# Performance work log

Hardware: AMD Instinct MI355X
Metric: run time of the kernel (lower is better)

Reference implementation:

```python
import jax, jax.numpy as jnp
import numpy as np

N = 50000          # nodes
E = 800000         # edges
D_IN, D_HID, D_OUT = 256, 128, 64
NUM_GRAPHS = 16
BN_EPS = 1e-5


def gcn_conv(x, src, dst, W, b, n_nodes):
    """PyG GCNConv: add self-loops, sym-normalized aggregation, then bias."""
    loop = jnp.arange(n_nodes, dtype=src.dtype)
    s = jnp.concatenate([src, loop])
    d = jnp.concatenate([dst, loop])
    deg = jax.ops.segment_sum(jnp.ones_like(s, dtype=x.dtype), d, num_segments=n_nodes)
    dinv = jax.lax.rsqrt(jnp.maximum(deg, 1.0))  # deg >= 1 due to self-loops
    norm = dinv[s] * dinv[d]                      # [E+N]
    h = x @ W                                     # [N, out]
    msg = h[s] * norm[:, None]                    # gather + scale
    out = jax.ops.segment_sum(msg, d, num_segments=n_nodes)
    return out + b


def batch_norm(x, gamma, beta):
    mu = jnp.mean(x, axis=0)
    var = jnp.mean(jnp.square(x - mu), axis=0)
    return (x - mu) * jax.lax.rsqrt(var + BN_EPS) * gamma + beta


def setup_inputs() -> dict:
    key = jax.random.key(0)
    ks = jax.random.split(key, 10)
    x = jax.random.normal(ks[0], (N, D_IN), dtype=jnp.float32)
    edge_index = jax.random.randint(ks[1], (2, E), 0, N, dtype=jnp.int64)
    batch = jnp.sort(jax.random.randint(ks[2], (N,), 0, NUM_GRAPHS, dtype=jnp.int64))
    def glorot(k, fan_in, fan_out):
        lim = np.sqrt(6.0 / (fan_in + fan_out))
        return jax.random.uniform(k, (fan_in, fan_out), jnp.float32, -lim, lim)
    return {
        "x": x, "edge_index": edge_index, "batch": batch,
        "W1": glorot(ks[3], D_IN, D_HID),  "b1": jnp.zeros((D_HID,), jnp.float32),
        "W2": glorot(ks[4], D_HID, D_HID), "b2": jnp.zeros((D_HID,), jnp.float32),
        "W3": glorot(ks[5], D_HID, D_OUT), "b3": jnp.zeros((D_OUT,), jnp.float32),
        "g1": jnp.ones((D_HID,), jnp.float32), "be1": jnp.zeros((D_HID,), jnp.float32),
        "g2": jnp.ones((D_HID,), jnp.float32), "be2": jnp.zeros((D_HID,), jnp.float32),
    }


def reference(x, edge_index, batch, W1, b1, W2, b2, W3, b3, g1, be1, g2, be2):
    src, dst = edge_index[0], edge_index[1]
    n = x.shape[0]
    h = gcn_conv(x, src, dst, W1, b1, n)
    h = jax.nn.relu(batch_norm(h, g1, be1))
    h = gcn_conv(h, src, dst, W2, b2, n)
    h = jax.nn.relu(batch_norm(h, g2, be2))
    h = gcn_conv(h, src, dst, W3, b3, n)          # [N, D_OUT]
    # global mean pool over graph ids
    sums = jax.ops.segment_sum(h, batch, num_segments=NUM_GRAPHS)
    cnts = jax.ops.segment_sum(jnp.ones((n,), h.dtype), batch, num_segments=NUM_GRAPHS)
    return sums / jnp.maximum(cnts, 1.0)[:, None]  # [NUM_GRAPHS, D_OUT]
```

## Files before the change

### kernel.cpp

```cpp
#include <hip/hip_runtime.h>
#include <hip/hip_bf16.h>

#define D_IN   256
#define D_HID  128
#define D_OUT_ 64
#define NGRAPH 16
#define BN_EPS 1e-5f

#define SCAN_TPB 256
#define SCAN_VPT 4

typedef __attribute__((ext_vector_type(8))) short short8;
typedef __attribute__((ext_vector_type(4))) float floatx4;

__device__ __forceinline__ unsigned short f2bf(float x) {
    unsigned u = __float_as_uint(x);
    return (unsigned short)((u + 0x7fffu + ((u >> 16) & 1u)) >> 16);
}
__device__ __forceinline__ unsigned pack2bf(float lo, float hi) {
    return (unsigned)f2bf(lo) | ((unsigned)f2bf(hi) << 16);
}
__device__ __forceinline__ void bf2_decode(unsigned u, float& lo, float& hi) {
    lo = __uint_as_float(u << 16);
    hi = __uint_as_float(u & 0xffff0000u);
}
__device__ __forceinline__ void accum8(float* acc, uint4 qv, float wt) {
    float f0,f1,f2,f3,f4,f5,f6,f7;
    bf2_decode(qv.x, f0, f1); bf2_decode(qv.y, f2, f3);
    bf2_decode(qv.z, f4, f5); bf2_decode(qv.w, f6, f7);
    acc[0]=fmaf(f0,wt,acc[0]); acc[1]=fmaf(f1,wt,acc[1]);
    acc[2]=fmaf(f2,wt,acc[2]); acc[3]=fmaf(f3,wt,acc[3]);
    acc[4]=fmaf(f4,wt,acc[4]); acc[5]=fmaf(f5,wt,acc[5]);
    acc[6]=fmaf(f6,wt,acc[6]); acc[7]=fmaf(f7,wt,acc[7]);
}

__global__ void count_rank_kernel(const int* __restrict__ dst, int E,
                                  int* __restrict__ deg, int* __restrict__ rank) {
    int e0 = blockIdx.x * (256 * 4) + threadIdx.x;
    int d[4];
    #pragma unroll
    for (int i = 0; i < 4; ++i) {
        int e = e0 + i * 256;
        if (e < E) d[i] = dst[e];
    }
    #pragma unroll
    for (int i = 0; i < 4; ++i) {
        int e = e0 + i * 256;
        if (e < E) rank[e] = atomicAdd(&deg[d[i]], 1);
    }
}

__global__ void dinv_bsum_kernel(const int* __restrict__ deg, int N,
                                 float* __restrict__ dinv, int* __restrict__ bsum) {
    __shared__ int red[SCAN_TPB];
    int t = threadIdx.x;
    int base = blockIdx.x * (SCAN_TPB * SCAN_VPT) + t;
    int s = 0;
    #pragma unroll
    for (int i = 0; i < SCAN_VPT; ++i) {
        int idx = base + i * SCAN_TPB;
        if (idx < N) {
            int d = deg[idx];
            dinv[idx] = rsqrtf((float)(d + 1));
            s += d;
        }
    }
    red[t] = s;
    __syncthreads();
    for (int off = SCAN_TPB / 2; off > 0; off >>= 1) {
        if (t < off) red[t] += red[t + off];
        __syncthreads();
    }
    if (t == 0) bsum[blockIdx.x] = red[0];
}

__global__ void scan_bsum_kernel(const int* __restrict__ bsum, int NB,
                                 int* __restrict__ bprefix,
                                 int* __restrict__ rowstart, int N, int E) {
    __shared__ int part[SCAN_TPB];
    int t = threadIdx.x;
    int s = (t < NB) ? bsum[t] : 0;
    part[t] = s;
    __syncthreads();
    for (int off = 1; off < SCAN_TPB; off <<= 1) {
        int x = (t >= off) ? part[t - off] : 0;
        __syncthreads();
        part[t] += x;
        __syncthreads();
    }
    if (t < NB) bprefix[t] = part[t] - s;
    if (t == 0) rowstart[N] = E;
}

__global__ void local_scan_kernel(const int* __restrict__ deg, int N,
                                  const int* __restrict__ bprefix,
                                  int* __restrict__ rowstart) {
    __shared__ int part[SCAN_TPB];
    int t = threadIdx.x;
    int base = blockIdx.x * (SCAN_TPB * SCAN_VPT) + t * SCAN_VPT;
    int v[SCAN_VPT];
    int s = 0;
    #pragma unroll
    for (int i = 0; i < SCAN_VPT; ++i) {
        v[i] = (base + i < N) ? deg[base + i] : 0;
        s += v[i];
    }
    part[t] = s;
    __syncthreads();
    for (int off = 1; off < SCAN_TPB; off <<= 1) {
        int x = (t >= off) ? part[t - off] : 0;
        __syncthreads();
        part[t] += x;
        __syncthreads();
    }
    int excl = part[t] - s + bprefix[blockIdx.x];
    #pragma unroll
    for (int i = 0; i < SCAN_VPT; ++i) {
        if (base + i < N) rowstart[base + i] = excl;
        excl += v[i];
    }
}

__global__ void scatter_kernel(const int* __restrict__ src, const int* __restrict__ dst,
                               int E, const int* __restrict__ rowstart,
                               const int* __restrict__ rank, int* __restrict__ csr) {
    int e0 = blockIdx.x * (256 * 4) + threadIdx.x;
    int d[4], rk[4], sv[4], pos[4];
    #pragma unroll
    for (int i = 0; i < 4; ++i) {
        int e = e0 + i * 256;
        if (e < E) { d[i] = dst[e]; rk[i] = rank[e]; sv[i] = src[e]; }
    }
    #pragma unroll
    for (int i = 0; i < 4; ++i) {
        int e = e0 + i * 256;
        if (e < E) pos[i] = rowstart[d[i]];
    }
    #pragma unroll
    for (int i = 0; i < 4; ++i) {
        int e = e0 + i * 256;
        if (e < E) csr[pos[i] + rk[i]] = sv[i];
    }
}

__global__ void wprep_all_kernel(const float* __restrict__ W1, const float* __restrict__ W2,
                                 const float* __restrict__ W3,
                                 unsigned short* __restrict__ Wt1,
                                 unsigned short* __restrict__ Wt2,
                                 unsigned short* __restrict__ Wt3) {
    int idx = blockIdx.x * blockDim.x + threadIdx.x;
    const int S1 = D_IN * D_HID;
    const int S2 = D_HID * D_HID;
    const int S3 = D_HID * D_OUT_;
    if (idx < S1) {
        int k = idx / D_HID, n = idx - k * D_HID;
        Wt1[(size_t)n * D_IN + k] = f2bf(W1[idx]);
    } else if (idx < S1 + S2) {
        int i = idx - S1;
        int k = i / D_HID, n = i - k * D_HID;
        Wt2[(size_t)n * D_HID + k] = f2bf(W2[i]);
    } else if (idx < S1 + S2 + S3) {
        int i = idx - S1 - S2;
        int k = i / D_OUT_, n = i - k * D_OUT_;
        Wt3[(size_t)n * D_HID + k] = f2bf(W3[i]);
    }
}

template<int K, int NOUT, int FUSE, int ABF16>
__device__ __forceinline__ void gemm_body(
        int bid, const void* __restrict__ Aptr, const unsigned short* __restrict__ Wt,
        unsigned short* __restrict__ Cb, int M,
        const float* __restrict__ sums, const float* __restrict__ sumsq,
        const float* __restrict__ gam, const float* __restrict__ bet, float invN) {
    constexpr int NT = NOUT / 16;
    constexpr int KS = K / 32;
    constexpr int CHUNKS = NOUT * K / 8;
    constexpr int KROW16 = K / 8;
    __shared__ unsigned short s_wt[NOUT * K];
    __shared__ float s_sc[FUSE ? K : 1];
    __shared__ float s_sh[FUSE ? K : 1];

    int lane = threadIdx.x & 63;
    int wave = threadIdx.x >> 6;
    int col  = lane & 15;
    int quad = lane >> 4;
    int kq   = quad * 8;
    int row  = bid * 64 + wave * 16 + col;
    int rowc = min(row, M - 1);

    uint4  qa[ABF16 ? KS : 1];
    float4 a0[ABF16 ? 1 : KS], a1[ABF16 ? 1 : KS];
    if (ABF16) {
        const unsigned short* Ab = (const unsigned short*)Aptr;
        #pragma unroll
        for (int i = 0; i < KS; ++i)
            qa[i] = *(const uint4*)&Ab[(size_t)rowc * K + i * 32 + kq];
    } else {
        const float* Af = (const float*)Aptr;
        #pragma unroll
        for (int i = 0; i < KS; ++i) {
            a0[i] = *(const float4*)&Af[(size_t)rowc * K + i * 32 + kq];
            a1[i] = *(const float4*)&Af[(size_t)rowc * K + i * 32 + kq + 4];
        }
    }

    {
        const uint4* Wg = (const uint4*)Wt;
        #pragma unroll
        for (int it = 0; it < CHUNKS / 256; ++it) {
            int c = it * 256 + (int)threadIdx.x;
            uint4 v = Wg[c];
            int n = c / KROW16;
            unsigned byte = ((unsigned)c * 16u) ^ ((unsigned)(n & 7) << 4);
            *(uint4*)((char*)s_wt + byte) = v;
        }
    }
    if (FUSE) {
        int t = threadIdx.x;
        if (t < K) {
            float mu  = sums[t] * invN;
            float var = sumsq[t] * invN - mu * mu;
            float sc  = gam[t] * rsqrtf(var + BN_EPS);
            s_sc[t] = sc;
            s_sh[t] = fmaf(-mu, sc, bet[t]);
        }
    }
    __syncthreads();

    short8 afr[KS];
    if (ABF16) {
        #pragma unroll
        for (int i = 0; i < KS; ++i) {
            if (FUSE) {
                int kb = i * 32 + kq;
                float f0,f1,f2,f3,f4,f5,f6,f7;
                bf2_decode(qa[i].x, f0, f1); bf2_decode(qa[i].y, f2, f3);
                bf2_decode(qa[i].z, f4, f5); bf2_decode(qa[i].w, f6, f7);
                float4 sc0 = *(const float4*)&s_sc[kb];
                float4 sc1 = *(const float4*)&s_sc[kb + 4];
                float4 sh0 = *(const float4*)&s_sh[kb];
                float4 sh1 = *(const float4*)&s_sh[kb + 4];
                f0 = fmaxf(0.f, fmaf(f0, sc0.x, sh0.x));
                f1 = fmaxf(0.f, fmaf(f1, sc0.y, sh0.y));
                f2 = fmaxf(0.f, fmaf(f2, sc0.z, sh0.z));
                f3 = fmaxf(0.f, fmaf(f3, sc0.w, sh0.w));
                f4 = fmaxf(0.f, fmaf(f4, sc1.x, sh1.x));
                f5 = fmaxf(0.f, fmaf(f5, sc1.y, sh1.y));
                f6 = fmaxf(0.f, fmaf(f6, sc1.z, sh1.z));
                f7 = fmaxf(0.f, fmaf(f7, sc1.w, sh1.w));
                uint4 p;
                p.x = pack2bf(f0, f1); p.y = pack2bf(f2, f3);
                p.z = pack2bf(f4, f5); p.w = pack2bf(f6, f7);
                afr[i] = __builtin_bit_cast(short8, p);
            } else {
                afr[i] = __builtin_bit_cast(short8, qa[i]);
            }
        }
    } else {
        #pragma unroll
        for (int i = 0; i < KS; ++i) {
            uint4 p;
            p.x = pack2bf(a0[i].x, a0[i].y); p.y = pack2bf(a0[i].z, a0[i].w);
            p.z = pack2bf(a1[i].x, a1[i].y); p.w = pack2bf(a1[i].z, a1[i].w);
            afr[i] = __builtin_bit_cast(short8, p);
        }
    }

    floatx4 acc[NT];
    #pragma unroll
    for (int nt = 0; nt < NT; ++nt) acc[nt] = (floatx4){0.f, 0.f, 0.f, 0.f};

    #pragma unroll
    for (int i = 0; i < KS; ++i) {
        #pragma unroll
        for (int nt = 0; nt < NT; ++nt) {
            unsigned byte = ((unsigned)((nt * 16 + col) * K + i * 32 + kq)) * 2u;
            byte ^= (unsigned)(col & 7) << 4;
            short8 bfrag = *(const short8*)((const char*)s_wt + byte);
            acc[nt] = __builtin_amdgcn_mfma_f32_16x16x32_bf16(afr[i], bfrag, acc[nt], 0, 0, 0);
        }
    }

    int obase = bid * 64 + wave * 16 + quad * 4;
    #pragma unroll
    for (int r = 0; r < 4; ++r) {
        int orow = obase + r;
        if (orow < M) {
            #pragma unroll
            for (int nt = 0; nt < NT; ++nt)
                Cb[(size_t)orow * NOUT + nt * 16 + col] = f2bf(acc[nt][r]);
        }
    }
}

template<int K, int NOUT, int FUSE, int ABF16>
__global__ __launch_bounds__(256, 2) void gemm_mfma_kernel(
        const void* __restrict__ Aptr, const unsigned short* __restrict__ Wt,
        unsigned short* __restrict__ Cb, int M,
        const float* __restrict__ sums, const float* __restrict__ sumsq,
        const float* __restrict__ gam, const float* __restrict__ bet, float invN) {
    gemm_body<K, NOUT, FUSE, ABF16>(blockIdx.x, Aptr, Wt, Cb, M, sums, sumsq, gam, bet, invN);
}

template<int D>
__global__ __launch_bounds__(256) void agg_bf16_kernel(
        const unsigned short* __restrict__ h, const float* __restrict__ dinv,
        const int* __restrict__ rowstart, const int* __restrict__ csr,
        const float* __restrict__ bias,
        unsigned short* __restrict__ outb, int N) {
    constexpr int LPR = D / 8;
    constexpr int RPB = 256 / LPR;
    int lane = threadIdx.x & (LPR - 1);
    int r    = threadIdx.x / LPR;
    int v = blockIdx.x * RPB + r;
    if (v >= N) return;
    int c0 = lane * 8;
    const unsigned short* hc = h + c0;
    float dv = dinv[v];

    float acc[8];
    {
        float w = dv * dv;
        uint4 q = *(const uint4*)&hc[(size_t)v * D];
        float4 b0 = *(const float4*)&bias[c0];
        float4 b1 = *(const float4*)&bias[c0 + 4];
        acc[0]=b0.x; acc[1]=b0.y; acc[2]=b0.z; acc[3]=b0.w;
        acc[4]=b1.x; acc[5]=b1.y; acc[6]=b1.z; acc[7]=b1.w;
        accum8(acc, q, w);
    }

    int j  = rowstart[v];
    int j1 = rowstart[v + 1];
    for (; j + 8 <= j1; j += 8) {
        int   s[8]; float w[8]; uint4 q[8];
        #pragma unroll
        for (int i = 0; i < 8; ++i) s[i] = csr[j + i];
        #pragma unroll
        for (int i = 0; i < 8; ++i) q[i] = *(const uint4*)&hc[(size_t)s[i] * D];
        #pragma unroll
        for (int i = 0; i < 8; ++i) w[i] = dinv[s[i]] * dv;
        #pragma unroll
        for (int i = 0; i < 8; ++i) accum8(acc, q[i], w[i]);
    }
    for (; j + 4 <= j1; j += 4) {
        int s0 = csr[j],     s1 = csr[j + 1];
        int s2 = csr[j + 2], s3 = csr[j + 3];
        float w0 = dinv[s0] * dv, w1 = dinv[s1] * dv;
        float w2 = dinv[s2] * dv, w3 = dinv[s3] * dv;
        uint4 q0 = *(const uint4*)&hc[(size_t)s0 * D];
        uint4 q1 = *(const uint4*)&hc[(size_t)s1 * D];
        uint4 q2 = *(const uint4*)&hc[(size_t)s2 * D];
        uint4 q3 = *(const uint4*)&hc[(size_t)s3 * D];
        accum8(acc, q0, w0); accum8(acc, q1, w1);
        accum8(acc, q2, w2); accum8(acc, q3, w3);
    }
    for (; j < j1; ++j) {
        int s = csr[j];
        float w = dinv[s] * dv;
        uint4 q = *(const uint4*)&hc[(size_t)s * D];
        accum8(acc, q, w);
    }

    uint4 o;
    o.x = pack2bf(acc[0], acc[1]); o.y = pack2bf(acc[2], acc[3]);
    o.z = pack2bf(acc[4], acc[5]); o.w = pack2bf(acc[6], acc[7]);
    *(uint4*)&outb[(size_t)v * D + c0] = o;
}

__global__ void bn_stats_bf16_kernel(const unsigned short* __restrict__ x, int N,
                                     float* __restrict__ sums, float* __restrict__ sumsq) {
    __shared__ float ls0[256], ls1[256], lq0[256], lq1[256];
    int pr = threadIdx.x & 63;
    int rg = threadIdx.x >> 6;
    float s0=0.f, s1=0.f, q0=0.f, q1=0.f;
    for (int v = blockIdx.x * 4 + rg; v < N; v += gridDim.x * 4) {
        unsigned u = *(const unsigned*)&x[(size_t)v * 128 + pr * 2];
        float lo, hi; bf2_decode(u, lo, hi);
        s0 += lo; s1 += hi;
        q0 = fmaf(lo, lo, q0); q1 = fmaf(hi, hi, q1);
    }
    ls0[threadIdx.x]=s0; ls1[threadIdx.x]=s1; lq0[threadIdx.x]=q0; lq1[threadIdx.x]=q1;
    __syncthreads();
    if (threadIdx.x < 64) {
        int pp = threadIdx.x;
        float a0=0,a1=0,b0=0,b1=0;
        #pragma unroll
        for (int g = 0; g < 4; ++g) {
            a0 += ls0[g*64+pp]; a1 += ls1[g*64+pp];
            b0 += lq0[g*64+pp]; b1 += lq1[g*64+pp];
        }
        atomicAdd(&sums[pp*2],  a0); atomicAdd(&sums[pp*2+1],  a1);
        atomicAdd(&sumsq[pp*2], b0); atomicAdd(&sumsq[pp*2+1], b1);
    }
}

__global__ void pool_bf16_kernel(const unsigned short* __restrict__ x,
                                 const int* __restrict__ batch, int N,
                                 float* __restrict__ psum, int* __restrict__ pcnt) {
    __shared__ float ls[NGRAPH * 64];
    __shared__ int   lc[NGRAPH];
    for (int i = threadIdx.x; i < NGRAPH * 64; i += blockDim.x) ls[i] = 0.f;
    if (threadIdx.x < NGRAPH) lc[threadIdx.x] = 0;
    __syncthreads();
    int total = N * 32;
    for (int idx = blockIdx.x * blockDim.x + threadIdx.x; idx < total;
         idx += gridDim.x * blockDim.x) {
        int v = idx >> 5, cp = idx & 31;
        unsigned u = *(const unsigned*)&x[(size_t)v * 64 + cp * 2];
        float lo, hi; bf2_decode(u, lo, hi);
        int g = batch[v];
        atomicAdd(&ls[g * 64 + cp * 2],     lo);
        atomicAdd(&ls[g * 64 + cp * 2 + 1], hi);
        if (cp == 0) atomicAdd(&lc[g], 1);
    }
    __syncthreads();
    for (int i = threadIdx.x; i < NGRAPH * 64; i += blockDim.x) atomicAdd(&psum[i], ls[i]);
    if (threadIdx.x < NGRAPH) atomicAdd(&pcnt[threadIdx.x], lc[threadIdx.x]);
}

__global__ void pool_final_kernel(const float* __restrict__ psum, const int* __restrict__ pcnt,
                                  float* __restrict__ out) {
    int i = threadIdx.x;
    int g = i >> 6;
    float cnt = (float)max(pcnt[g], 1);
    out[i] = psum[i] / cnt;
}

extern "C" void kernel_launch(void* const* d_in, const int* in_sizes, int n_in,
                              void* d_out, int out_size, void* d_ws, size_t ws_size,
                              hipStream_t stream) {
    const float* x   = (const float*)d_in[0];
    const int*   ei  = (const int*)d_in[1];
    const int*   bat = (const int*)d_in[2];
    const float* W1  = (const float*)d_in[3];
    const float* b1  = (const float*)d_in[4];
    const float* W2  = (const float*)d_in[5];
    const float* b2  = (const float*)d_in[6];
    const float* W3  = (const float*)d_in[7];
    const float* b3  = (const float*)d_in[8];
    const float* g1  = (const float*)d_in[9];
    const float* be1 = (const float*)d_in[10];
    const float* g2  = (const float*)d_in[11];
    const float* be2 = (const float*)d_in[12];
    float* out = (float*)d_out;

    int N = in_sizes[0] / D_IN;
    int E = in_sizes[1] / 2;
    const int* src = ei;
    const int* dst = ei + E;

    char* p = (char*)d_ws;
    auto alloc = [&](size_t bytes) { char* r = p; p += (bytes + 255) & ~(size_t)255; return r; };
    int NB = (N + SCAN_TPB * SCAN_VPT - 1) / (SCAN_TPB * SCAN_VPT);
    char*  zbase    = p;
    int*   deg      = (int*)  alloc((size_t)N * 4);
    float* sums1    = (float*)alloc(128 * 4);
    float* sumsq1   = (float*)alloc(128 * 4);
    float* sums2    = (float*)alloc(128 * 4);
    float* sumsq2   = (float*)alloc(128 * 4);
    float* psum     = (float*)alloc(NGRAPH * 64 * 4);
    int*   pcnt     = (int*)  alloc(NGRAPH * 4);
    size_t zspan    = (size_t)(p - zbase);
    int*   rowstart = (int*)  alloc((size_t)(N + 1) * 4);
    int*   rank     = (int*)  alloc((size_t)E * 4);
    float* dinv     = (float*)alloc((size_t)N * 4);
    int*   bsum     = (int*)  alloc((size_t)NB * 4);
    int*   bprefix  = (int*)  alloc((size_t)NB * 4);
    int*   csr      = (int*)  alloc((size_t)E * 4);
    unsigned short* hb16   = (unsigned short*)alloc((size_t)N * 128 * 2);
    unsigned short* aggb16 = (unsigned short*)alloc((size_t)N * 128 * 2);
    unsigned short* Wt1 = (unsigned short*)alloc((size_t)D_HID * D_IN * 2);
    unsigned short* Wt2 = (unsigned short*)alloc((size_t)D_HID * D_HID * 2);
    unsigned short* Wt3 = (unsigned short*)alloc((size_t)D_OUT_ * D_HID * 2);

    int ebl4 = (E + 1023) / 1024;
    int gblocks = (N + 63) / 64;
    float invN = 1.0f / (float)N;
    int wtot = D_IN * D_HID + D_HID * D_HID + D_HID * D_OUT_;

    (void)hipMemsetAsync(zbase, 0, zspan, stream);
    wprep_all_kernel<<<(wtot + 255) / 256, 256, 0, stream>>>(W1, W2, W3, Wt1, Wt2, Wt3);

    count_rank_kernel<<<ebl4, 256, 0, stream>>>(dst, E, deg, rank);
    dinv_bsum_kernel<<<NB, SCAN_TPB, 0, stream>>>(deg, N, dinv, bsum);
    scan_bsum_kernel<<<1, SCAN_TPB, 0, stream>>>(bsum, NB, bprefix, rowstart, N, E);
    local_scan_kernel<<<NB, SCAN_TPB, 0, stream>>>(deg, N, bprefix, rowstart);
    scatter_kernel<<<ebl4, 256, 0, stream>>>(src, dst, E, rowstart, rank, csr);

    gemm_mfma_kernel<D_IN, D_HID, 0, 0><<<gblocks, 256, 0, stream>>>(
        x, Wt1, hb16, N, nullptr, nullptr, nullptr, nullptr, 0.f);

    agg_bf16_kernel<D_HID><<<(N + 15) / 16, 256, 0, stream>>>(
        hb16, dinv, rowstart, csr, b1, aggb16, N);
    bn_stats_bf16_kernel<<<256, 256, 0, stream>>>(aggb16, N, sums1, sumsq1);

    gemm_mfma_kernel<D_HID, D_HID, 1, 1><<<gblocks, 256, 0, stream>>>(
        aggb16, Wt2, hb16, N, sums1, sumsq1, g1, be1, invN);
    agg_bf16_kernel<D_HID><<<(N + 15) / 16, 256, 0, stream>>>(
        hb16, dinv, rowstart, csr, b2, aggb16, N);
    bn_stats_bf16_kernel<<<256, 256, 0, stream>>>(aggb16, N, sums2, sumsq2);

    gemm_mfma_kernel<D_HID, D_OUT_, 1, 1><<<gblocks, 256, 0, stream>>>(
        aggb16, Wt3, hb16, N, sums2, sumsq2, g2, be2, invN);
    agg_bf16_kernel<D_OUT_><<<(N + 31) / 32, 256, 0, stream>>>(
        hb16, dinv, rowstart, csr, b3, aggb16, N);

    pool_bf16_kernel<<<256, 256, 0, stream>>>(aggb16, bat, N, psum, pcnt);
    pool_final_kernel<<<1, NGRAPH * 64, 0, stream>>>(psum, pcnt, out);
}
```

Baseline: 357.0 us.

## Fuse CSR build, BN stats and pooling into neighbouring kernels

Weight prep is merged with degree counting in one launch. The per-edge rank array is replaced by an atomic cursor, and that scatter shares a launch with the first GEMM. BN statistics and global mean pooling move into the aggregation kernels' epilogues, so the separate stats and pool passes and the final bf16 output write are dropped. This cuts launches and memory re-reads, but CSR neighbour order becomes nondeterministic, which changes float summation order, and more global atomics are added per block.

```diff
diff --git a/kernel.cpp b/kernel.cpp
--- a/kernel.cpp
+++ b/kernel.cpp
@@ -34,19 +34,43 @@
     acc[6]=fmaf(f6,wt,acc[6]); acc[7]=fmaf(f7,wt,acc[7]);
 }
 
-__global__ void count_rank_kernel(const int* __restrict__ dst, int E,
-                                  int* __restrict__ deg, int* __restrict__ rank) {
-    int e0 = blockIdx.x * (256 * 4) + threadIdx.x;
-    int d[4];
-    #pragma unroll
-    for (int i = 0; i < 4; ++i) {
-        int e = e0 + i * 256;
-        if (e < E) d[i] = dst[e];
-    }
-    #pragma unroll
-    for (int i = 0; i < 4; ++i) {
-        int e = e0 + i * 256;
-        if (e < E) rank[e] = atomicAdd(&deg[d[i]], 1);
+__global__ void prep_count_kernel(const float* __restrict__ W1, const float* __restrict__ W2,
+                                  const float* __restrict__ W3,
+                                  unsigned short* __restrict__ Wt1,
+                                  unsigned short* __restrict__ Wt2,
+                                  unsigned short* __restrict__ Wt3, int WB,
+                                  const int* __restrict__ dst, int E,
+                                  int* __restrict__ deg) {
+    if ((int)blockIdx.x < WB) {
+        int idx = blockIdx.x * 256 + threadIdx.x;
+        const int S1 = D_IN * D_HID;
+        const int S2 = D_HID * D_HID;
+        const int S3 = D_HID * D_OUT_;
+        if (idx < S1) {
+            int k = idx / D_HID, n = idx - k * D_HID;
+            Wt1[(size_t)n * D_IN + k] = f2bf(W1[idx]);
+        } else if (idx < S1 + S2) {
+            int i = idx - S1;
+            int k = i / D_HID, n = i - k * D_HID;
+            Wt2[(size_t)n * D_HID + k] = f2bf(W2[i]);
+        } else if (idx < S1 + S2 + S3) {
+            int i = idx - S1 - S2;
+            int k = i / D_OUT_, n = i - k * D_OUT_;
+            Wt3[(size_t)n * D_HID + k] = f2bf(W3[i]);
+        }
+    } else {
+        int e0 = ((int)blockIdx.x - WB) * (256 * 4) + threadIdx.x;
+        int d[4];
+        #pragma unroll
+        for (int i = 0; i < 4; ++i) {
+            int e = e0 + i * 256;
+            if (e < E) d[i] = dst[e];
+        }
+        #pragma unroll
+        for (int i = 0; i < 4; ++i) {
+            int e = e0 + i * 256;
+            if (e < E) atomicAdd(&deg[d[i]], 1);
+        }
     }
 }
 
@@ -94,7 +118,7 @@
 
 __global__ void local_scan_kernel(const int* __restrict__ deg, int N,
                                   const int* __restrict__ bprefix,
-                                  int* __restrict__ rowstart) {
+                                  int* __restrict__ rowstart, int* __restrict__ cursor) {
     __shared__ int part[SCAN_TPB];
     int t = threadIdx.x;
     int base = blockIdx.x * (SCAN_TPB * SCAN_VPT) + t * SCAN_VPT;
@@ -116,53 +140,8 @@
     int excl = part[t] - s + bprefix[blockIdx.x];
     #pragma unroll
     for (int i = 0; i < SCAN_VPT; ++i) {
-        if (base + i < N) rowstart[base + i] = excl;
+        if (base + i < N) { rowstart[base + i] = excl; cursor[base + i] = excl; }
         excl += v[i];
-    }
-}
-
-__global__ void scatter_kernel(const int* __restrict__ src, const int* __restrict__ dst,
-                               int E, const int* __restrict__ rowstart,
-                               const int* __restrict__ rank, int* __restrict__ csr) {
-    int e0 = blockIdx.x * (256 * 4) + threadIdx.x;
-    int d[4], rk[4], sv[4], pos[4];
-    #pragma unroll
-    for (int i = 0; i < 4; ++i) {
-        int e = e0 + i * 256;
-        if (e < E) { d[i] = dst[e]; rk[i] = rank[e]; sv[i] = src[e]; }
-    }
-    #pragma unroll
-    for (int i = 0; i < 4; ++i) {
-        int e = e0 + i * 256;
-        if (e < E) pos[i] = rowstart[d[i]];
-    }
-    #pragma unroll
-    for (int i = 0; i < 4; ++i) {
-        int e = e0 + i * 256;
-        if (e < E) csr[pos[i] + rk[i]] = sv[i];
-    }
-}
-
-__global__ void wprep_all_kernel(const float* __restrict__ W1, const float* __restrict__ W2,
-                                 const float* __restrict__ W3,
-                                 unsigned short* __restrict__ Wt1,
-                                 unsigned short* __restrict__ Wt2,
-                                 unsigned short* __restrict__ Wt3) {
-    int idx = blockIdx.x * blockDim.x + threadIdx.x;
-    const int S1 = D_IN * D_HID;
-    const int S2 = D_HID * D_HID;
-    const int S3 = D_HID * D_OUT_;
-    if (idx < S1) {
-        int k = idx / D_HID, n = idx - k * D_HID;
-        Wt1[(size_t)n * D_IN + k] = f2bf(W1[idx]);
-    } else if (idx < S1 + S2) {
-        int i = idx - S1;
-        int k = i / D_HID, n = i - k * D_HID;
-        Wt2[(size_t)n * D_HID + k] = f2bf(W2[i]);
-    } else if (idx < S1 + S2 + S3) {
-        int i = idx - S1 - S2;
-        int k = i / D_OUT_, n = i - k * D_OUT_;
-        Wt3[(size_t)n * D_HID + k] = f2bf(W3[i]);
     }
 }
 
@@ -302,26 +281,71 @@
     gemm_body<K, NOUT, FUSE, ABF16>(blockIdx.x, Aptr, Wt, Cb, M, sums, sumsq, gam, bet, invN);
 }
 
-template<int D>
+__global__ __launch_bounds__(256, 2) void gemm1_scatter_kernel(
+        const float* __restrict__ x, const unsigned short* __restrict__ Wt1,
+        unsigned short* __restrict__ Cb, int M, int GB,
+        const int* __restrict__ src, const int* __restrict__ dst, int E,
+        int* __restrict__ cursor, int* __restrict__ csr) {
+    if ((int)blockIdx.x < GB) {
+        gemm_body<D_IN, D_HID, 0, 0>(blockIdx.x, x, Wt1, Cb, M,
+                                     nullptr, nullptr, nullptr, nullptr, 0.f);
+    } else {
+        int e0 = ((int)blockIdx.x - GB) * (256 * 4) + threadIdx.x;
+        int d[4], sv[4];
+        #pragma unroll
+        for (int i = 0; i < 4; ++i) {
+            int e = e0 + i * 256;
+            if (e < E) { d[i] = dst[e]; sv[i] = src[e]; }
+        }
+        #pragma unroll
+        for (int i = 0; i < 4; ++i) {
+            int e = e0 + i * 256;
+            if (e < E) {
+                int pos = atomicAdd(&cursor[d[i]], 1);
+                csr[pos] = sv[i];
+            }
+        }
+    }
+}
+
+template<int D, int BNS, int POOL>
 __global__ __launch_bounds__(256) void agg_bf16_kernel(
         const unsigned short* __restrict__ h, const float* __restrict__ dinv,
         const int* __restrict__ rowstart, const int* __restrict__ csr,
         const float* __restrict__ bias,
-        unsigned short* __restrict__ outb, int N) {
+        unsigned short* __restrict__ outb, int N,
+        float* __restrict__ sums, float* __restrict__ sumsq,
+        const int* __restrict__ batch, float* __restrict__ psum,
+        int* __restrict__ pcnt) {
+    static_assert(!BNS || D == 128, "BNS reduce assumes LPR=16 (4 rows/wave)");
     constexpr int LPR = D / 8;
     constexpr int RPB = 256 / LPR;
+    __shared__ float s_ps[BNS ? 4 : 1][BNS ? 128 : 1];
+    __shared__ float s_pq[BNS ? 4 : 1][BNS ? 128 : 1];
+    __shared__ float s_pool[POOL ? NGRAPH : 1][POOL ? 64 : 1];
+    __shared__ int   s_cnt[POOL ? NGRAPH : 1];
+    __shared__ int   s_gmin, s_gmax;
+
+    if (POOL) {
+        for (int i = threadIdx.x; i < NGRAPH * 64; i += 256) (&s_pool[0][0])[i] = 0.f;
+        if (threadIdx.x < NGRAPH) s_cnt[threadIdx.x] = 0;
+        if (threadIdx.x == 0) { s_gmin = NGRAPH - 1; s_gmax = 0; }
+        __syncthreads();
+    }
+
     int lane = threadIdx.x & (LPR - 1);
     int r    = threadIdx.x / LPR;
     int v = blockIdx.x * RPB + r;
-    if (v >= N) return;
+    bool valid = v < N;
+    int vc = valid ? v : N - 1;
     int c0 = lane * 8;
     const unsigned short* hc = h + c0;
-    float dv = dinv[v];
+    float dv = dinv[vc];
 
     float acc[8];
     {
         float w = dv * dv;
-        uint4 q = *(const uint4*)&hc[(size_t)v * D];
+        uint4 q = *(const uint4*)&hc[(size_t)vc * D];
         float4 b0 = *(const float4*)&bias[c0];
         float4 b1 = *(const float4*)&bias[c0 + 4];
         acc[0]=b0.x; acc[1]=b0.y; acc[2]=b0.z; acc[3]=b0.w;
@@ -329,8 +353,8 @@
         accum8(acc, q, w);
     }
 
-    int j  = rowstart[v];
-    int j1 = rowstart[v + 1];
+    int j  = rowstart[vc];
+    int j1 = valid ? rowstart[vc + 1] : j;
     for (; j + 8 <= j1; j += 8) {
         int   s[8]; float w[8]; uint4 q[8];
         #pragma unroll
@@ -361,61 +385,63 @@
         accum8(acc, q, w);
     }
 
-    uint4 o;
-    o.x = pack2bf(acc[0], acc[1]); o.y = pack2bf(acc[2], acc[3]);
-    o.z = pack2bf(acc[4], acc[5]); o.w = pack2bf(acc[6], acc[7]);
-    *(uint4*)&outb[(size_t)v * D + c0] = o;
-}
-
-__global__ void bn_stats_bf16_kernel(const unsigned short* __restrict__ x, int N,
-                                     float* __restrict__ sums, float* __restrict__ sumsq) {
-    __shared__ float ls0[256], ls1[256], lq0[256], lq1[256];
-    int pr = threadIdx.x & 63;
-    int rg = threadIdx.x >> 6;
-    float s0=0.f, s1=0.f, q0=0.f, q1=0.f;
-    for (int v = blockIdx.x * 4 + rg; v < N; v += gridDim.x * 4) {
-        unsigned u = *(const unsigned*)&x[(size_t)v * 128 + pr * 2];
-        float lo, hi; bf2_decode(u, lo, hi);
-        s0 += lo; s1 += hi;
-        q0 = fmaf(lo, lo, q0); q1 = fmaf(hi, hi, q1);
-    }
-    ls0[threadIdx.x]=s0; ls1[threadIdx.x]=s1; lq0[threadIdx.x]=q0; lq1[threadIdx.x]=q1;
-    __syncthreads();
-    if (threadIdx.x < 64) {
-        int pp = threadIdx.x;
-        float a0=0,a1=0,b0=0,b1=0;
-        #pragma unroll
-        for (int g = 0; g < 4; ++g) {
-            a0 += ls0[g*64+pp]; a1 += ls1[g*64+pp];
-            b0 += lq0[g*64+pp]; b1 += lq1[g*64+pp];
-        }
-        atomicAdd(&sums[pp*2],  a0); atomicAdd(&sums[pp*2+1],  a1);
-        atomicAdd(&sumsq[pp*2], b0); atomicAdd(&sumsq[pp*2+1], b1);
-    }
-}
-
-__global__ void pool_bf16_kernel(const unsigned short* __restrict__ x,
-                                 const int* __restrict__ batch, int N,
-                                 float* __restrict__ psum, int* __restrict__ pcnt) {
-    __shared__ float ls[NGRAPH * 64];
-    __shared__ int   lc[NGRAPH];
-    for (int i = threadIdx.x; i < NGRAPH * 64; i += blockDim.x) ls[i] = 0.f;
-    if (threadIdx.x < NGRAPH) lc[threadIdx.x] = 0;
-    __syncthreads();
-    int total = N * 32;
-    for (int idx = blockIdx.x * blockDim.x + threadIdx.x; idx < total;
-         idx += gridDim.x * blockDim.x) {
-        int v = idx >> 5, cp = idx & 31;
-        unsigned u = *(const unsigned*)&x[(size_t)v * 64 + cp * 2];
-        float lo, hi; bf2_decode(u, lo, hi);
-        int g = batch[v];
-        atomicAdd(&ls[g * 64 + cp * 2],     lo);
-        atomicAdd(&ls[g * 64 + cp * 2 + 1], hi);
-        if (cp == 0) atomicAdd(&lc[g], 1);
-    }
-    __syncthreads();
-    for (int i = threadIdx.x; i < NGRAPH * 64; i += blockDim.x) atomicAdd(&psum[i], ls[i]);
-    if (threadIdx.x < NGRAPH) atomicAdd(&pcnt[threadIdx.x], lc[threadIdx.x]);
+    if (!POOL && valid) {
+        uint4 o;
+        o.x = pack2bf(acc[0], acc[1]); o.y = pack2bf(acc[2], acc[3]);
+        o.z = pack2bf(acc[4], acc[5]); o.w = pack2bf(acc[6], acc[7]);
+        *(uint4*)&outb[(size_t)v * D + c0] = o;
+    }
+
+    if (BNS) {
+        float s[8], q2[8];
+        #pragma unroll
+        for (int i = 0; i < 8; ++i) {
+            s[i]  = valid ? acc[i] : 0.f;
+            q2[i] = valid ? acc[i] * acc[i] : 0.f;
+        }
+        #pragma unroll
+        for (int i = 0; i < 8; ++i) {
+            s[i]  += __shfl_xor(s[i], 16);  s[i]  += __shfl_xor(s[i], 32);
+            q2[i] += __shfl_xor(q2[i], 16); q2[i] += __shfl_xor(q2[i], 32);
+        }
+        int wv = threadIdx.x >> 6;
+        if ((threadIdx.x & 48) == 0) {
+            int l = threadIdx.x & 15;
+            #pragma unroll
+            for (int i = 0; i < 8; ++i) {
+                s_ps[wv][l * 8 + i] = s[i];
+                s_pq[wv][l * 8 + i] = q2[i];
+            }
+        }
+        __syncthreads();
+        int t = threadIdx.x;
+        if (t < 128) {
+            float vv = s_ps[0][t] + s_ps[1][t] + s_ps[2][t] + s_ps[3][t];
+            atomicAdd(&sums[t], vv);
+        } else {
+            int ch = t - 128;
+            float vv = s_pq[0][ch] + s_pq[1][ch] + s_pq[2][ch] + s_pq[3][ch];
+            atomicAdd(&sumsq[ch], vv);
+        }
+    }
+
+    if (POOL) {
+        if (valid) {
+            int g = batch[v];
+            #pragma unroll
+            for (int i = 0; i < 8; ++i) atomicAdd(&s_pool[g][c0 + i], acc[i]);
+            if (lane == 0) {
+                atomicAdd(&s_cnt[g], 1);
+                atomicMin(&s_gmin, g);
+                atomicMax(&s_gmax, g);
+            }
+        }
+        __syncthreads();
+        for (int g = s_gmin; g <= s_gmax; ++g)
+            if (threadIdx.x < 64) atomicAdd(&psum[g * 64 + threadIdx.x], s_pool[g][threadIdx.x]);
+        if (threadIdx.x < NGRAPH && s_cnt[threadIdx.x] > 0)
+            atomicAdd(&pcnt[threadIdx.x], s_cnt[threadIdx.x]);
+    }
 }
 
 __global__ void pool_final_kernel(const float* __restrict__ psum, const int* __restrict__ pcnt,
@@ -462,7 +488,7 @@
     int*   pcnt     = (int*)  alloc(NGRAPH * 4);
     size_t zspan    = (size_t)(p - zbase);
     int*   rowstart = (int*)  alloc((size_t)(N + 1) * 4);
-    int*   rank     = (int*)  alloc((size_t)E * 4);
+    int*   cursor   = (int*)  alloc((size_t)N * 4);
     float* dinv     = (float*)alloc((size_t)N * 4);
     int*   bsum     = (int*)  alloc((size_t)NB * 4);
     int*   bprefix  = (int*)  alloc((size_t)NB * 4);
@@ -477,34 +503,31 @@
     int gblocks = (N + 63) / 64;
     float invN = 1.0f / (float)N;
     int wtot = D_IN * D_HID + D_HID * D_HID + D_HID * D_OUT_;
+    int WB = (wtot + 255) / 256;
 
     (void)hipMemsetAsync(zbase, 0, zspan, stream);
-    wprep_all_kernel<<<(wtot + 255) / 256, 256, 0, stream>>>(W1, W2, W3, Wt1, Wt2, Wt3);
-
-    count_rank_kernel<<<ebl4, 256, 0, stream>>>(dst, E, deg, rank);
+    prep_count_kernel<<<WB + ebl4, 256, 0, stream>>>(W1, W2, W3, Wt1, Wt2, Wt3,
+                                                     WB, dst, E, deg);
+
     dinv_bsum_kernel<<<NB, SCAN_TPB, 0, stream>>>(deg, N, dinv, bsum);
     scan_bsum_kernel<<<1, SCAN_TPB, 0, stream>>>(bsum, NB, bprefix, rowstart, N, E);
-    local_scan_kernel<<<NB, SCAN_TPB, 0, stream>>>(deg, N, bprefix, rowstart);
-    scatter_kernel<<<ebl4, 256, 0, stream>>>(src, dst, E, rowstart, rank, csr);
-
-    gemm_mfma_kernel<D_IN, D_HID, 0, 0><<<gblocks, 256, 0, stream>>>(
-        x, Wt1, hb16, N, nullptr, nullptr, nullptr, nullptr, 0.f);
-
-    agg_bf16_kernel<D_HID><<<(N + 15) / 16, 256, 0, stream>>>(
-        hb16, dinv, rowstart, csr, b1, aggb16, N);
-    bn_stats_bf16_kernel<<<256, 256, 0, stream>>>(aggb16, N, sums1, sumsq1);
+    local_scan_kernel<<<NB, SCAN_TPB, 0, stream>>>(deg, N, bprefix, rowstart, cursor);
+
+    gemm1_scatter_kernel<<<gblocks + ebl4, 256, 0, stream>>>(
+        x, Wt1, hb16, N, gblocks, src, dst, E, cursor, csr);
+
+    agg_bf16_kernel<D_HID, 1, 0><<<(N + 15) / 16, 256, 0, stream>>>(
+        hb16, dinv, rowstart, csr, b1, aggb16, N, sums1, sumsq1, nullptr, nullptr, nullptr);
 
     gemm_mfma_kernel<D_HID, D_HID, 1, 1><<<gblocks, 256, 0, stream>>>(
         aggb16, Wt2, hb16, N, sums1, sumsq1, g1, be1, invN);
-    agg_bf16_kernel<D_HID><<<(N + 15) / 16, 256, 0, stream>>>(
-        hb16, dinv, rowstart, csr, b2, aggb16, N);
-    bn_stats_bf16_kernel<<<256, 256, 0, stream>>>(aggb16, N, sums2, sumsq2);
+    agg_bf16_kernel<D_HID, 1, 0><<<(N + 15) / 16, 256, 0, stream>>>(
+        hb16, dinv, rowstart, csr, b2, aggb16, N, sums2, sumsq2, nullptr, nullptr, nullptr);
 
     gemm_mfma_kernel<D_HID, D_OUT_, 1, 1><<<gblocks, 256, 0, stream>>>(
         aggb16, Wt3, hb16, N, sums2, sumsq2, g2, be2, invN);
-    agg_bf16_kernel<D_OUT_><<<(N + 31) / 32, 256, 0, stream>>>(
-        hb16, dinv, rowstart, csr, b3, aggb16, N);
-
-    pool_bf16_kernel<<<256, 256, 0, stream>>>(aggb16, bat, N, psum, pcnt);
+    agg_bf16_kernel<D_OUT_, 0, 1><<<(N + 31) / 32, 256, 0, stream>>>(
+        hb16, dinv, rowstart, csr, b3, nullptr, N, nullptr, nullptr, bat, psum, pcnt);
+
     pool_final_kernel<<<1, NGRAPH * 64, 0, stream>>>(psum, pcnt, out);
 }
```

New measurement: 466.5 us. 30.7% more time.

## Fuse weight prep with degree count and overlap CSR scatter with first GEMM

Applied to the files above, without the earlier changes.

Merges the weight transpose/convert kernel with the degree-count kernel into one launch, and merges the CSR scatter with the first GEMM through block-index partitioning so the two independent stages run concurrently. The scatter now takes positions from a per-node atomic cursor initialised from the scan, so the per-edge rank array and its extra read and write pass are gone. This removes two kernel launches and some memory traffic. In exchange, the order of neighbours within each CSR row becomes nondeterministic, which changes floating-point summation order, and the scatter blocks must share the GPU with GEMM blocks that run at launch bounds (256,2).

```diff
diff --git a/kernel.cpp b/kernel.cpp
--- a/kernel.cpp
+++ b/kernel.cpp
@@ -34,19 +34,43 @@
     acc[6]=fmaf(f6,wt,acc[6]); acc[7]=fmaf(f7,wt,acc[7]);
 }
 
-__global__ void count_rank_kernel(const int* __restrict__ dst, int E,
-                                  int* __restrict__ deg, int* __restrict__ rank) {
-    int e0 = blockIdx.x * (256 * 4) + threadIdx.x;
-    int d[4];
-    #pragma unroll
-    for (int i = 0; i < 4; ++i) {
-        int e = e0 + i * 256;
-        if (e < E) d[i] = dst[e];
-    }
-    #pragma unroll
-    for (int i = 0; i < 4; ++i) {
-        int e = e0 + i * 256;
-        if (e < E) rank[e] = atomicAdd(&deg[d[i]], 1);
+__global__ void prep_count_kernel(const float* __restrict__ W1, const float* __restrict__ W2,
+                                  const float* __restrict__ W3,
+                                  unsigned short* __restrict__ Wt1,
+                                  unsigned short* __restrict__ Wt2,
+                                  unsigned short* __restrict__ Wt3, int WB,
+                                  const int* __restrict__ dst, int E,
+                                  int* __restrict__ deg) {
+    if ((int)blockIdx.x < WB) {
+        int idx = blockIdx.x * 256 + threadIdx.x;
+        const int S1 = D_IN * D_HID;
+        const int S2 = D_HID * D_HID;
+        const int S3 = D_HID * D_OUT_;
+        if (idx < S1) {
+            int k = idx / D_HID, n = idx - k * D_HID;
+            Wt1[(size_t)n * D_IN + k] = f2bf(W1[idx]);
+        } else if (idx < S1 + S2) {
+            int i = idx - S1;
+            int k = i / D_HID, n = i - k * D_HID;
+            Wt2[(size_t)n * D_HID + k] = f2bf(W2[i]);
+        } else if (idx < S1 + S2 + S3) {
+            int i = idx - S1 - S2;
+            int k = i / D_OUT_, n = i - k * D_OUT_;
+            Wt3[(size_t)n * D_HID + k] = f2bf(W3[i]);
+        }
+    } else {
+        int e0 = ((int)blockIdx.x - WB) * (256 * 4) + threadIdx.x;
+        int d[4];
+        #pragma unroll
+        for (int i = 0; i < 4; ++i) {
+            int e = e0 + i * 256;
+            if (e < E) d[i] = dst[e];
+        }
+        #pragma unroll
+        for (int i = 0; i < 4; ++i) {
+            int e = e0 + i * 256;
+            if (e < E) atomicAdd(&deg[d[i]], 1);
+        }
     }
 }
 
@@ -94,7 +118,7 @@
 
 __global__ void local_scan_kernel(const int* __restrict__ deg, int N,
                                   const int* __restrict__ bprefix,
-                                  int* __restrict__ rowstart) {
+                                  int* __restrict__ rowstart, int* __restrict__ cursor) {
     __shared__ int part[SCAN_TPB];
     int t = threadIdx.x;
     int base = blockIdx.x * (SCAN_TPB * SCAN_VPT) + t * SCAN_VPT;
@@ -116,53 +140,8 @@
     int excl = part[t] - s + bprefix[blockIdx.x];
     #pragma unroll
     for (int i = 0; i < SCAN_VPT; ++i) {
-        if (base + i < N) rowstart[base + i] = excl;
+        if (base + i < N) { rowstart[base + i] = excl; cursor[base + i] = excl; }
         excl += v[i];
-    }
-}
-
-__global__ void scatter_kernel(const int* __restrict__ src, const int* __restrict__ dst,
-                               int E, const int* __restrict__ rowstart,
-                               const int* __restrict__ rank, int* __restrict__ csr) {
-    int e0 = blockIdx.x * (256 * 4) + threadIdx.x;
-    int d[4], rk[4], sv[4], pos[4];
-    #pragma unroll
-    for (int i = 0; i < 4; ++i) {
-        int e = e0 + i * 256;
-        if (e < E) { d[i] = dst[e]; rk[i] = rank[e]; sv[i] = src[e]; }
-    }
-    #pragma unroll
-    for (int i = 0; i < 4; ++i) {
-        int e = e0 + i * 256;
-        if (e < E) pos[i] = rowstart[d[i]];
-    }
-    #pragma unroll
-    for (int i = 0; i < 4; ++i) {
-        int e = e0 + i * 256;
-        if (e < E) csr[pos[i] + rk[i]] = sv[i];
-    }
-}
-
-__global__ void wprep_all_kernel(const float* __restrict__ W1, const float* __restrict__ W2,
-                                 const float* __restrict__ W3,
-                                 unsigned short* __restrict__ Wt1,
-                                 unsigned short* __restrict__ Wt2,
-                                 unsigned short* __restrict__ Wt3) {
-    int idx = blockIdx.x * blockDim.x + threadIdx.x;
-    const int S1 = D_IN * D_HID;
-    const int S2 = D_HID * D_HID;
-    const int S3 = D_HID * D_OUT_;
-    if (idx < S1) {
-        int k = idx / D_HID, n = idx - k * D_HID;
-        Wt1[(size_t)n * D_IN + k] = f2bf(W1[idx]);
-    } else if (idx < S1 + S2) {
-        int i = idx - S1;
-        int k = i / D_HID, n = i - k * D_HID;
-        Wt2[(size_t)n * D_HID + k] = f2bf(W2[i]);
-    } else if (idx < S1 + S2 + S3) {
-        int i = idx - S1 - S2;
-        int k = i / D_OUT_, n = i - k * D_OUT_;
-        Wt3[(size_t)n * D_HID + k] = f2bf(W3[i]);
     }
 }
 
@@ -302,6 +281,33 @@
     gemm_body<K, NOUT, FUSE, ABF16>(blockIdx.x, Aptr, Wt, Cb, M, sums, sumsq, gam, bet, invN);
 }
 
+__global__ __launch_bounds__(256, 2) void gemm1_scatter_kernel(
+        const float* __restrict__ x, const unsigned short* __restrict__ Wt1,
+        unsigned short* __restrict__ Cb, int M, int GB,
+        const int* __restrict__ src, const int* __restrict__ dst, int E,
+        int* __restrict__ cursor, int* __restrict__ csr) {
+    if ((int)blockIdx.x < GB) {
+        gemm_body<D_IN, D_HID, 0, 0>(blockIdx.x, x, Wt1, Cb, M,
+                                     nullptr, nullptr, nullptr, nullptr, 0.f);
+    } else {
+        int e0 = ((int)blockIdx.x - GB) * (256 * 4) + threadIdx.x;
+        int d[4], sv[4];
+        #pragma unroll
+        for (int i = 0; i < 4; ++i) {
+            int e = e0 + i * 256;
+            if (e < E) { d[i] = dst[e]; sv[i] = src[e]; }
+        }
+        #pragma unroll
+        for (int i = 0; i < 4; ++i) {
+            int e = e0 + i * 256;
+            if (e < E) {
+                int pos = atomicAdd(&cursor[d[i]], 1);
+                csr[pos] = sv[i];
+            }
+        }
+    }
+}
+
 template<int D>
 __global__ __launch_bounds__(256) void agg_bf16_kernel(
         const unsigned short* __restrict__ h, const float* __restrict__ dinv,
@@ -462,7 +468,7 @@
     int*   pcnt     = (int*)  alloc(NGRAPH * 4);
     size_t zspan    = (size_t)(p - zbase);
     int*   rowstart = (int*)  alloc((size_t)(N + 1) * 4);
-    int*   rank     = (int*)  alloc((size_t)E * 4);
+    int*   cursor   = (int*)  alloc((size_t)N * 4);
     float* dinv     = (float*)alloc((size_t)N * 4);
     int*   bsum     = (int*)  alloc((size_t)NB * 4);
     int*   bprefix  = (int*)  alloc((size_t)NB * 4);
@@ -477,18 +483,18 @@
     int gblocks = (N + 63) / 64;
     float invN = 1.0f / (float)N;
     int wtot = D_IN * D_HID + D_HID * D_HID + D_HID * D_OUT_;
+    int WB = (wtot + 255) / 256;
 
     (void)hipMemsetAsync(zbase, 0, zspan, stream);
-    wprep_all_kernel<<<(wtot + 255) / 256, 256, 0, stream>>>(W1, W2, W3, Wt1, Wt2, Wt3);
-
-    count_rank_kernel<<<ebl4, 256, 0, stream>>>(dst, E, deg, rank);
+    prep_count_kernel<<<WB + ebl4, 256, 0, stream>>>(W1, W2, W3, Wt1, Wt2, Wt3,
+                                                     WB, dst, E, deg);
+
     dinv_bsum_kernel<<<NB, SCAN_TPB, 0, stream>>>(deg, N, dinv, bsum);
     scan_bsum_kernel<<<1, SCAN_TPB, 0, stream>>>(bsum, NB, bprefix, rowstart, N, E);
-    local_scan_kernel<<<NB, SCAN_TPB, 0, stream>>>(deg, N, bprefix, rowstart);
-    scatter_kernel<<<ebl4, 256, 0, stream>>>(src, dst, E, rowstart, rank, csr);
-
-    gemm_mfma_kernel<D_IN, D_HID, 0, 0><<<gblocks, 256, 0, stream>>>(
-        x, Wt1, hb16, N, nullptr, nullptr, nullptr, nullptr, 0.f);
+    local_scan_kernel<<<NB, SCAN_TPB, 0, stream>>>(deg, N, bprefix, rowstart, cursor);
+
+    gemm1_scatter_kernel<<<gblocks + ebl4, 256, 0, stream>>>(
+        x, Wt1, hb16, N, gblocks, src, dst, E, cursor, csr);
 
     agg_bf16_kernel<D_HID><<<(N + 15) / 16, 256, 0, stream>>>(
         hb16, dinv, rowstart, csr, b1, aggb16, N);
```

Result: slower. 384.8 us (+7.8%).
